# Kernel optimization log

Hardware: AMD Instinct MI355X
Metric: run time of the kernel (lower is better)

## Reference

```python
import math
import jax, jax.numpy as jnp
import numpy as np

B, S, D, H = 2, 2048, 1024, 16
DH = D // H
DFF = 4 * D
EPS = 1e-6
MASKED_BIAS = -10000.0


def _gelu(x):
    # GPT-2 tanh-approx GELU
    return 0.5 * x * (1.0 + jnp.tanh(math.sqrt(2.0 / math.pi) * (x + 0.044715 * x ** 3)))


def _layernorm(x, w, b):
    mean = jnp.mean(x, axis=-1, keepdims=True)
    var = jnp.mean((x - mean) ** 2, axis=-1, keepdims=True)
    return w * ((x - mean) / jnp.sqrt(var + EPS)) + b


def setup_inputs() -> dict:
    key = jax.random.key(0)
    ks = jax.random.split(key, 6)
    std = 0.02
    return {
        "hidden_states": jax.random.normal(ks[0], (B, S, D), jnp.float32),
        "w_attn": jax.random.normal(ks[1], (D, 3 * D), jnp.float32) * std,
        "b_attn": jnp.zeros((3 * D,), jnp.float32),
        "w_proj": jax.random.normal(ks[2], (D, D), jnp.float32) * std,
        "b_proj": jnp.zeros((D,), jnp.float32),
        "w_fc": jax.random.normal(ks[3], (D, DFF), jnp.float32) * std,
        "b_fc": jnp.zeros((DFF,), jnp.float32),
        "w_fc_proj": jax.random.normal(ks[4], (DFF, D), jnp.float32) * std,
        "b_fc_proj": jnp.zeros((D,), jnp.float32),
        "ln1_w": jnp.ones((D,), jnp.float32),
        "ln1_b": jnp.zeros((D,), jnp.float32),
        "ln2_w": jnp.ones((D,), jnp.float32),
        "ln2_b": jnp.zeros((D,), jnp.float32),
    }


def reference(hidden_states, w_attn, b_attn, w_proj, b_proj, w_fc, b_fc,
              w_fc_proj, b_fc_proj, ln1_w, ln1_b, ln2_w, ln2_b):
    residual = hidden_states
    x = _layernorm(hidden_states, ln1_w, ln1_b)

    # c_attn: [B,S,D] @ [D,3D] + b -> split into q,k,v
    qkv = x @ w_attn + b_attn
    q, k, v = jnp.split(qkv, 3, axis=-1)
    # split heads -> [B,H,S,DH]
    q = q.reshape(B, S, H, DH).transpose(0, 2, 1, 3)
    k = k.reshape(B, S, H, DH).transpose(0, 2, 1, 3)
    v = v.reshape(B, S, H, DH).transpose(0, 2, 1, 3)

    scores = jnp.einsum('bhqd,bhkd->bhqk', q, k) / jnp.sqrt(jnp.float32(DH))
    causal = jnp.tril(jnp.ones((S, S), bool))  # [S,S]
    scores = jnp.where(causal[None, None], scores, jnp.float32(MASKED_BIAS))
    attn = jax.nn.softmax(scores, axis=-1)
    out = jnp.einsum('bhqk,bhkd->bhqd', attn, v)
    out = out.transpose(0, 2, 1, 3).reshape(B, S, D)
    out = out @ w_proj + b_proj

    h = residual + out
    residual = h
    y = _layernorm(h, ln2_w, ln2_b)
    y = _gelu(y @ w_fc + b_fc)
    y = y @ w_fc_proj + b_fc_proj
    return residual + y
```

## Files before the change

kernel.cpp:

```cpp
#include <hip/hip_runtime.h>
#include <cstdint>
#include <cstddef>

typedef unsigned short u16;
typedef float  floatx4 __attribute__((ext_vector_type(4)));
typedef short  short8  __attribute__((ext_vector_type(8)));
typedef u16    usx4    __attribute__((ext_vector_type(4)));
typedef u16    usx8    __attribute__((ext_vector_type(8)));

__device__ __forceinline__ u16 f2b(float f) {
  unsigned u = __float_as_uint(f);
  unsigned r = u + 0x7fffu + ((u >> 16) & 1u);
  return (u16)(r >> 16);
}
__device__ __forceinline__ float b2f(u16 s) {
  return __uint_as_float(((unsigned)s) << 16);
}

__device__ __forceinline__ float gelu_f(float x) {
  const float c = 0.7978845608028654f;
  float t = tanhf(c * (x + 0.044715f * x * x * x));
  return 0.5f * x * (1.0f + t);
}

__device__ __forceinline__ void gl2lds16(const u16* g, u16* l) {
  __builtin_amdgcn_global_load_lds(
      (const __attribute__((address_space(1))) unsigned int*)g,
      (__attribute__((address_space(3))) unsigned int*)l, 16, 0, 0);
}

__global__ __launch_bounds__(256) void ln_bf16_kernel(
    const float* __restrict__ in, const float* __restrict__ w,
    const float* __restrict__ b, u16* __restrict__ out)
{
  const int row = blockIdx.x;
  const int t = threadIdx.x;
  const float* p = in + (size_t)row * 1024 + t * 4;
  floatx4 v = *(const floatx4*)p;
  float s  = v.x + v.y + v.z + v.w;
  float ss = v.x*v.x + v.y*v.y + v.z*v.z + v.w*v.w;
  #pragma unroll
  for (int m = 1; m < 64; m <<= 1) {
    s  += __shfl_xor(s,  m);
    ss += __shfl_xor(ss, m);
  }
  __shared__ float red[8];
  if ((t & 63) == 0) { red[(t >> 6)*2] = s; red[(t >> 6)*2 + 1] = ss; }
  __syncthreads();
  s  = red[0] + red[2] + red[4] + red[6];
  ss = red[1] + red[3] + red[5] + red[7];
  const float mean = s * (1.0f / 1024.0f);
  const float var  = ss * (1.0f / 1024.0f) - mean * mean;
  const float rstd = rsqrtf(var + 1e-6f);
  floatx4 wv = *(const floatx4*)(w + t * 4);
  floatx4 bv = *(const floatx4*)(b + t * 4);
  usx4 o = { f2b(wv.x * ((v.x - mean) * rstd) + bv.x),
             f2b(wv.y * ((v.y - mean) * rstd) + bv.y),
             f2b(wv.z * ((v.z - mean) * rstd) + bv.z),
             f2b(wv.w * ((v.w - mean) * rstd) + bv.w) };
  *(usx4*)(out + (size_t)row * 1024 + t * 4) = o;
}

__global__ __launch_bounds__(256) void wtrans_kernel(
    const float* __restrict__ in, u16* __restrict__ out, int K, int N)
{
  __shared__ u16 tile[32][33];
  const int n0 = blockIdx.x * 32, k0 = blockIdx.y * 32;
  const int tx = threadIdx.x & 31, ty = threadIdx.x >> 5;
  #pragma unroll
  for (int i = 0; i < 4; ++i)
    tile[ty + i*8][tx] = f2b(in[(size_t)(k0 + ty + i*8) * N + n0 + tx]);
  __syncthreads();
  #pragma unroll
  for (int i = 0; i < 4; ++i)
    out[(size_t)(n0 + ty + i*8) * K + k0 + tx] = tile[tx][ty + i*8];
}

template<int BM, int BN, int FLAGS, int MINW>
__global__ __launch_bounds__(256, MINW) void gemm_mfma_kernel(
    const u16* __restrict__ A, const u16* __restrict__ Bt,
    const float* __restrict__ bias, const float* __restrict__ Res,
    void* __restrict__ Cout, int M, int N, int K, int kLen)
{
  constexpr int WM = BM / 2, WN = BN / 2;
  constexpr int MT = WM / 16, NT = WN / 16;
  __shared__ u16 As[BM * 32];
  __shared__ u16 Bs[BN * 32];

  const int t = threadIdx.x;
  const int wave = t >> 6, lane = t & 63;
  const int quad = lane >> 4, l16 = lane & 15;
  const int wm = wave >> 1, wn = wave & 1;
  const int bm0 = blockIdx.y * BM, bn0 = blockIdx.x * BN;
  const int kStart = blockIdx.z * kLen;

  const int sRow = lane >> 2;
  const int sq   = lane & 3;

  const u16* aG[BM / 64];
  u16* aL[BM / 64];
  #pragma unroll
  for (int j = 0; j < BM / 64; ++j) {
    const int band = j * 4 + wave;
    aG[j] = A + (size_t)(bm0 + band * 16 + sRow) * K + kStart + sq * 8;
    aL[j] = As + band * 512;
  }
  const u16* bG[BN / 64];
  u16* bL[BN / 64];
  #pragma unroll
  for (int j = 0; j < BN / 64; ++j) {
    const int band = j * 4 + wave;
    bG[j] = Bt + (size_t)(bn0 + band * 16 + sRow) * K + kStart + sq * 8;
    bL[j] = Bs + band * 512;
  }

  floatx4 acc[MT][NT] = {};

  for (int k0 = 0; k0 < kLen; k0 += 32) {
    __syncthreads();
    #pragma unroll
    for (int j = 0; j < BM / 64; ++j) gl2lds16(aG[j] + k0, aL[j]);
    #pragma unroll
    for (int j = 0; j < BN / 64; ++j) gl2lds16(bG[j] + k0, bL[j]);
    __syncthreads();

    short8 af[MT], bf[NT];
    #pragma unroll
    for (int mt = 0; mt < MT; ++mt)
      af[mt] = *(const short8*)&As[(wm*WM + mt*16 + l16) * 32 + quad * 8];
    #pragma unroll
    for (int nt = 0; nt < NT; ++nt)
      bf[nt] = *(const short8*)&Bs[(wn*WN + nt*16 + l16) * 32 + quad * 8];
    #pragma unroll
    for (int mt = 0; mt < MT; ++mt)
      #pragma unroll
      for (int nt = 0; nt < NT; ++nt)
        acc[mt][nt] = __builtin_amdgcn_mfma_f32_16x16x32_bf16(af[mt], bf[nt], acc[mt][nt], 0, 0, 0);
  }

  const int orow0 = bm0 + wm * WM;
  const int ocol0 = bn0 + wn * WN;
  const size_t zoff = (size_t)blockIdx.z * M * N;
  #pragma unroll
  for (int nt = 0; nt < NT; ++nt) {
    const int col = ocol0 + nt*16 + l16;
    const float bv = bias ? bias[col] : 0.0f;
    #pragma unroll
    for (int mt = 0; mt < MT; ++mt) {
      #pragma unroll
      for (int r = 0; r < 4; ++r) {
        const int row = orow0 + mt*16 + quad*4 + r;
        float v = acc[mt][nt][r] + bv;
        if (FLAGS & 1) v = gelu_f(v);
        if (FLAGS & 2) v += Res[(size_t)row * N + col];
        if (FLAGS & 4) ((u16*)Cout)[zoff + (size_t)row * N + col] = f2b(v);
        else           ((float*)Cout)[zoff + (size_t)row * N + col] = v;
      }
    }
  }
}

__global__ __launch_bounds__(256, 4) void attn_mfma_kernel(
    const u16* __restrict__ qkv, u16* __restrict__ opart, float* __restrict__ ml)
{
  __shared__ u16 Ks[64][72];
  __shared__ u16 Vt[64][72];
  __shared__ u16 Ps[64][72];

  const int t    = threadIdx.x;
  const int wave = t >> 6;
  const int lane = t & 63;
  const int quad = lane >> 4;
  const int l16  = lane & 15;
  const int pair = blockIdx.x >> 1;
  const int half = blockIdx.x & 1;
  const int h    = blockIdx.y;
  const int b    = blockIdx.z;

  const size_t base = (size_t)b * 2048 * 3072;
  const int qoff = h * 64;
  const int koff = 1024 + h * 64;
  const int voff = 2048 + h * 64;

  const int srow = t >> 2;
  const int scol = (t & 3) * 16;
  const int kpair  = t & 31;
  const int vchunk = t >> 5;

  const size_t obase  = ((((size_t)half * 2 + b) * 16 + h) * 2048) * 64;
  const size_t mlbase = ((((size_t)half * 2 + b) * 16 + h) * 2048) * 2;

  const float C2 = 0.18033688011112042f;

  #pragma unroll 1
  for (int iter = 0; iter < 2; ++iter) {
    const int qi = iter ? (31 - pair) : pair;
    const int q0 = qi << 6;
    const int T  = qi + 1;
    const int mid = (T + 1) >> 1;
    const int t0 = half ? mid : 0;
    const int t1 = half ? T : mid;

    floatx4 of[4] = {};
    float m[4], l[4];
    #pragma unroll
    for (int r = 0; r < 4; ++r) { m[r] = -1e30f; l[r] = 0.f; }

    if (t0 < t1) {
      __syncthreads();
      {
        const u16* qp = qkv + base + (size_t)(q0 + srow) * 3072 + qoff + scol;
        *(usx8*)&Ks[srow][scol]     = *(const usx8*)qp;
        *(usx8*)&Ks[srow][scol + 8] = *(const usx8*)(qp + 8);
      }
      __syncthreads();
      const short8 qf0 = *(const short8*)&Ks[wave*16 + l16][quad*8];
      const short8 qf1 = *(const short8*)&Ks[wave*16 + l16][32 + quad*8];

      usx8 kr0, kr1, vr0, vr1;
      {
        const int k0 = t0 << 6;
        const u16* kp = qkv + base + (size_t)(k0 + srow) * 3072 + koff + scol;
        kr0 = *(const usx8*)kp; kr1 = *(const usx8*)(kp + 8);
        const u16* vp = qkv + base + (size_t)(k0 + 2*kpair) * 3072 + voff + vchunk*8;
        vr0 = *(const usx8*)vp; vr1 = *(const usx8*)(vp + 3072);
      }

      for (int tIdx = t0; tIdx < t1; ++tIdx) {
        __syncthreads();
        *(usx8*)&Ks[srow][scol]     = kr0;
        *(usx8*)&Ks[srow][scol + 8] = kr1;
        #pragma unroll
        for (int i = 0; i < 8; ++i)
          *(unsigned*)&Vt[vchunk*8 + i][2*kpair] =
              (unsigned)vr0[i] | ((unsigned)vr1[i] << 16);
        __syncthreads();

        if (tIdx + 1 < t1) {
          const int kn = (tIdx + 1) << 6;
          const u16* kp = qkv + base + (size_t)(kn + srow) * 3072 + koff + scol;
          kr0 = *(const usx8*)kp; kr1 = *(const usx8*)(kp + 8);
          const u16* vp = qkv + base + (size_t)(kn + 2*kpair) * 3072 + voff + vchunk*8;
          vr0 = *(const usx8*)vp; vr1 = *(const usx8*)(vp + 3072);
        }

        const int k0 = tIdx << 6;
        floatx4 sf[4];
        #pragma unroll
        for (int kt = 0; kt < 4; ++kt) {
          short8 kf0 = *(const short8*)&Ks[kt*16 + l16][quad*8];
          short8 kf1 = *(const short8*)&Ks[kt*16 + l16][32 + quad*8];
          floatx4 z = {};
          z      = __builtin_amdgcn_mfma_f32_16x16x32_bf16(qf0, kf0, z, 0, 0, 0);
          sf[kt] = __builtin_amdgcn_mfma_f32_16x16x32_bf16(qf1, kf1, z, 0, 0, 0);
        }

        const bool diag = (tIdx == qi);
        #pragma unroll
        for (int r = 0; r < 4; ++r) {
          const int qrow = q0 + wave*16 + quad*4 + r;
          float sv[4];
          #pragma unroll
          for (int kt = 0; kt < 4; ++kt) {
            sv[kt] = sf[kt][r] * C2;
            if (diag && (k0 + kt*16 + l16 > qrow)) sv[kt] = -1e30f;
          }
          float mx = fmaxf(fmaxf(sv[0], sv[1]), fmaxf(sv[2], sv[3]));
          #pragma unroll
          for (int msk = 1; msk < 16; msk <<= 1) mx = fmaxf(mx, __shfl_xor(mx, msk));
          const float nm = fmaxf(m[r], mx);
          float rs = 0.f;
          u16 pb[4];
          #pragma unroll
          for (int kt = 0; kt < 4; ++kt) {
            pb[kt] = f2b(exp2f(sv[kt] - nm));
            rs += b2f(pb[kt]);
          }
          #pragma unroll
          for (int msk = 1; msk < 16; msk <<= 1) rs += __shfl_xor(rs, msk);
          const float alpha = exp2f(m[r] - nm);
          m[r] = nm;
          l[r] = l[r] * alpha + rs;
          #pragma unroll
          for (int dht = 0; dht < 4; ++dht) of[dht][r] *= alpha;
          #pragma unroll
          for (int kt = 0; kt < 4; ++kt)
            Ps[wave*16 + quad*4 + r][kt*16 + l16] = pb[kt];
        }

        short8 pf0 = *(const short8*)&Ps[wave*16 + l16][quad*8];
        short8 pf1 = *(const short8*)&Ps[wave*16 + l16][32 + quad*8];
        #pragma unroll
        for (int dht = 0; dht < 4; ++dht) {
          short8 vf0 = *(const short8*)&Vt[dht*16 + l16][quad*8];
          short8 vf1 = *(const short8*)&Vt[dht*16 + l16][32 + quad*8];
          of[dht] = __builtin_amdgcn_mfma_f32_16x16x32_bf16(pf0, vf0, of[dht], 0, 0, 0);
          of[dht] = __builtin_amdgcn_mfma_f32_16x16x32_bf16(pf1, vf1, of[dht], 0, 0, 0);
        }
      }
    }

    #pragma unroll
    for (int r = 0; r < 4; ++r) {
      const int s = q0 + wave*16 + quad*4 + r;
      u16* orow = opart + obase + (size_t)s * 64;
      #pragma unroll
      for (int dht = 0; dht < 4; ++dht) orow[dht*16 + l16] = f2b(of[dht][r]);
      if (l16 == 0) { ml[mlbase + 2*s] = m[r]; ml[mlbase + 2*s + 1] = l[r]; }
    }
  }
}

__global__ __launch_bounds__(256) void attn_combine_kernel(
    const u16* __restrict__ opart, const float* __restrict__ ml,
    u16* __restrict__ out)
{
  const int t = threadIdx.x;
  const int s = blockIdx.x * 4 + (t >> 6);
  const int lane = t & 63;
  const int h = blockIdx.y, b = blockIdx.z;

  const size_t o0  = ((((size_t)0 * 2 + b) * 16 + h) * 2048 + s) * 64 + lane;
  const size_t o1  = ((((size_t)1 * 2 + b) * 16 + h) * 2048 + s) * 64 + lane;
  const size_t ml0 = ((((size_t)0 * 2 + b) * 16 + h) * 2048 + s) * 2;
  const size_t ml1 = ((((size_t)1 * 2 + b) * 16 + h) * 2048 + s) * 2;

  const float m0 = ml[ml0], l0 = ml[ml0 + 1];
  const float m1 = ml[ml1], l1 = ml[ml1 + 1];
  const float M  = fmaxf(m0, m1);
  const float w0 = exp2f(m0 - M), w1 = exp2f(m1 - M);
  const float L  = w0 * l0 + w1 * l1;
  const float o  = w0 * b2f(opart[o0]) + w1 * b2f(opart[o1]);
  out[((size_t)b * 2048 + s) * 1024 + h * 64 + lane] = f2b(o / L);
}

__global__ __launch_bounds__(256) void fcproj_combine_kernel(
    const u16* __restrict__ p, const float* __restrict__ hbuf,
    const float* __restrict__ bias, float* __restrict__ out)
{
  const size_t i0 = ((size_t)blockIdx.x * 256 + threadIdx.x) * 8;
  usx8 a = *(const usx8*)(p + i0);
  usx8 c = *(const usx8*)(p + 4194304 + i0);
  const int col = (int)(i0 & 1023);
  floatx4 bv0 = *(const floatx4*)(bias + col);
  floatx4 bv1 = *(const floatx4*)(bias + col + 4);
  floatx4 h0 = *(const floatx4*)(hbuf + i0);
  floatx4 h1 = *(const floatx4*)(hbuf + i0 + 4);
  floatx4 o0, o1;
  #pragma unroll
  for (int i = 0; i < 4; ++i) o0[i] = h0[i] + b2f(a[i])   + b2f(c[i])   + bv0[i];
  #pragma unroll
  for (int i = 0; i < 4; ++i) o1[i] = h1[i] + b2f(a[4+i]) + b2f(c[4+i]) + bv1[i];
  *(floatx4*)(out + i0)     = o0;
  *(floatx4*)(out + i0 + 4) = o1;
}

extern "C" void kernel_launch(void* const* d_in, const int* in_sizes, int n_in,
                              void* d_out, int out_size, void* d_ws, size_t ws_size,
                              hipStream_t stream) {
  const float* hidden    = (const float*)d_in[0];
  const float* w_attn    = (const float*)d_in[1];
  const float* b_attn    = (const float*)d_in[2];
  const float* w_proj    = (const float*)d_in[3];
  const float* b_proj    = (const float*)d_in[4];
  const float* w_fc      = (const float*)d_in[5];
  const float* b_fc      = (const float*)d_in[6];
  const float* w_fc_proj = (const float*)d_in[7];
  const float* b_fc_proj = (const float*)d_in[8];
  const float* ln1_w     = (const float*)d_in[9];
  const float* ln1_b     = (const float*)d_in[10];
  const float* ln2_w     = (const float*)d_in[11];
  const float* ln2_b     = (const float*)d_in[12];

  char* wsb = (char*)d_ws;
  u16*   xb    = (u16*)  (wsb + (size_t)( 0u << 20));
  u16*   qkvb  = (u16*)  (wsb + (size_t)( 8u << 20));
  u16*   attnb = (u16*)  (wsb + (size_t)(32u << 20));
  float* hbuf  = (float*)(wsb + (size_t)(40u << 20));
  u16*   opart = (u16*)  (wsb + (size_t)(40u << 20));
  float* mlbuf = (float*)(wsb + (size_t)(56u << 20));
  u16*   wqT   = (u16*)  (wsb + (size_t)(56u << 20));
  u16*   wpT   = (u16*)  (wsb + (size_t)(62u << 20));
  u16*   wfT   = (u16*)  (wsb + (size_t)(64u << 20));
  u16*   wfpT  = (u16*)  (wsb + (size_t)(72u << 20));
  u16*   pfcp  = (u16*)  (wsb + (size_t)(56u << 20));
  u16*   fcb   = qkvb;
  u16*   yb    = xb;

  wtrans_kernel<<<dim3(96, 32),  256, 0, stream>>>(w_attn,    wqT,  1024, 3072);
  wtrans_kernel<<<dim3(32, 32),  256, 0, stream>>>(w_proj,    wpT,  1024, 1024);
  wtrans_kernel<<<dim3(128, 32), 256, 0, stream>>>(w_fc,      wfT,  1024, 4096);
  wtrans_kernel<<<dim3(32, 128), 256, 0, stream>>>(w_fc_proj, wfpT, 4096, 1024);

  ln_bf16_kernel<<<4096, 256, 0, stream>>>(hidden, ln1_w, ln1_b, xb);
  gemm_mfma_kernel<128,128,4,4><<<dim3(24, 32, 1), 256, 0, stream>>>(
      xb, wqT, b_attn, nullptr, qkvb, 4096, 3072, 1024, 1024);
  attn_mfma_kernel<<<dim3(32, 16, 2), 256, 0, stream>>>(qkvb, opart, mlbuf);
  attn_combine_kernel<<<dim3(512, 16, 2), 256, 0, stream>>>(opart, mlbuf, attnb);
  gemm_mfma_kernel<128,64,2,4><<<dim3(16, 32, 1), 256, 0, stream>>>(
      attnb, wpT, b_proj, hidden, hbuf, 4096, 1024, 1024, 1024);
  ln_bf16_kernel<<<4096, 256, 0, stream>>>(hbuf, ln2_w, ln2_b, yb);
  gemm_mfma_kernel<256,128,5,2><<<dim3(32, 16, 1), 256, 0, stream>>>(
      yb, wfT, b_fc, nullptr, fcb, 4096, 4096, 1024, 1024);
  gemm_mfma_kernel<128,64,4,4><<<dim3(16, 32, 2), 256, 0, stream>>>(
      fcb, wfpT, nullptr, nullptr, pfcp, 4096, 1024, 4096, 2048);
  fcproj_combine_kernel<<<dim3(2048), 256, 0, stream>>>(pfcp, hbuf, b_fc_proj, (float*)d_out);
}
```

Measured before the change: 405.7 us.

## Fold softmax scale into QKV GEMM, compute row sums via MFMA, retile fc_proj

The Q-column scaling by log2(e)/sqrt(dh) moves into the QKV GEMM epilogue (flag 8), so the attention kernel no longer multiplies every score. The per-row softmax denominators are now accumulated by an extra MFMA of P against a ones vector, replacing the shuffle-reduced sum, and the max reduction uses width-16 shuffles. The fc_proj GEMM switches to 128x128 tiles with half as many column blocks. This trims VALU and cross-lane work in the attention inner loop at the cost of two extra MFMAs per tile and a small extra multiply in the GEMM epilogue.

```diff
diff --git a/kernel.cpp b/kernel.cpp
--- a/kernel.cpp
+++ b/kernel.cpp
@@ -28,6 +28,8 @@
       (const __attribute__((address_space(1))) unsigned int*)g,
       (__attribute__((address_space(3))) unsigned int*)l, 16, 0, 0);
 }
+
+#define C2SCALE 0.18033688011112042f
 
 __global__ __launch_bounds__(256) void ln_bf16_kernel(
     const float* __restrict__ in, const float* __restrict__ w,
@@ -145,6 +147,7 @@
   for (int nt = 0; nt < NT; ++nt) {
     const int col = ocol0 + nt*16 + l16;
     const float bv = bias ? bias[col] : 0.0f;
+    const float postscale = ((FLAGS & 8) && col < 1024) ? C2SCALE : 1.0f;
     #pragma unroll
     for (int mt = 0; mt < MT; ++mt) {
       #pragma unroll
@@ -152,6 +155,7 @@
         const int row = orow0 + mt*16 + quad*4 + r;
         float v = acc[mt][nt][r] + bv;
         if (FLAGS & 1) v = gelu_f(v);
+        if (FLAGS & 8) v *= postscale;
         if (FLAGS & 2) v += Res[(size_t)row * N + col];
         if (FLAGS & 4) ((u16*)Cout)[zoff + (size_t)row * N + col] = f2b(v);
         else           ((float*)Cout)[zoff + (size_t)row * N + col] = v;
@@ -190,7 +194,12 @@
   const size_t obase  = ((((size_t)half * 2 + b) * 16 + h) * 2048) * 64;
   const size_t mlbase = ((((size_t)half * 2 + b) * 16 + h) * 2048) * 2;
 
-  const float C2 = 0.18033688011112042f;
+  short8 onesb;
+  {
+    const short v = (l16 == 0) ? (short)0x3F80 : (short)0;
+    #pragma unroll
+    for (int i = 0; i < 8; ++i) onesb[i] = v;
+  }
 
   #pragma unroll 1
   for (int iter = 0; iter < 2; ++iter) {
@@ -202,9 +211,10 @@
     const int t1 = half ? T : mid;
 
     floatx4 of[4] = {};
-    float m[4], l[4];
-    #pragma unroll
-    for (int r = 0; r < 4; ++r) { m[r] = -1e30f; l[r] = 0.f; }
+    floatx4 ofl = {};
+    float m[4];
+    #pragma unroll
+    for (int r = 0; r < 4; ++r) m[r] = -1e30f;
 
     if (t0 < t1) {
       __syncthreads();
@@ -258,34 +268,27 @@
         const bool diag = (tIdx == qi);
         #pragma unroll
         for (int r = 0; r < 4; ++r) {
-          const int qrow = q0 + wave*16 + quad*4 + r;
-          float sv[4];
+          float sv0 = sf[0][r], sv1 = sf[1][r], sv2 = sf[2][r], sv3 = sf[3][r];
+          if (diag) {
+            const int qrow = q0 + wave*16 + quad*4 + r;
+            if (k0 +      l16 > qrow) sv0 = -1e30f;
+            if (k0 + 16 + l16 > qrow) sv1 = -1e30f;
+            if (k0 + 32 + l16 > qrow) sv2 = -1e30f;
+            if (k0 + 48 + l16 > qrow) sv3 = -1e30f;
+          }
+          float mx = fmaxf(fmaxf(sv0, sv1), fmaxf(sv2, sv3));
           #pragma unroll
-          for (int kt = 0; kt < 4; ++kt) {
-            sv[kt] = sf[kt][r] * C2;
-            if (diag && (k0 + kt*16 + l16 > qrow)) sv[kt] = -1e30f;
-          }
-          float mx = fmaxf(fmaxf(sv[0], sv[1]), fmaxf(sv[2], sv[3]));
-          #pragma unroll
-          for (int msk = 1; msk < 16; msk <<= 1) mx = fmaxf(mx, __shfl_xor(mx, msk));
+          for (int msk = 1; msk < 16; msk <<= 1) mx = fmaxf(mx, __shfl_xor(mx, msk, 16));
           const float nm = fmaxf(m[r], mx);
-          float rs = 0.f;
-          u16 pb[4];
-          #pragma unroll
-          for (int kt = 0; kt < 4; ++kt) {
-            pb[kt] = f2b(exp2f(sv[kt] - nm));
-            rs += b2f(pb[kt]);
-          }
-          #pragma unroll
-          for (int msk = 1; msk < 16; msk <<= 1) rs += __shfl_xor(rs, msk);
           const float alpha = exp2f(m[r] - nm);
           m[r] = nm;
-          l[r] = l[r] * alpha + rs;
+          Ps[wave*16 + quad*4 + r][     l16] = f2b(exp2f(sv0 - nm));
+          Ps[wave*16 + quad*4 + r][16 + l16] = f2b(exp2f(sv1 - nm));
+          Ps[wave*16 + quad*4 + r][32 + l16] = f2b(exp2f(sv2 - nm));
+          Ps[wave*16 + quad*4 + r][48 + l16] = f2b(exp2f(sv3 - nm));
           #pragma unroll
           for (int dht = 0; dht < 4; ++dht) of[dht][r] *= alpha;
-          #pragma unroll
-          for (int kt = 0; kt < 4; ++kt)
-            Ps[wave*16 + quad*4 + r][kt*16 + l16] = pb[kt];
+          ofl[r] *= alpha;
         }
 
         short8 pf0 = *(const short8*)&Ps[wave*16 + l16][quad*8];
@@ -297,6 +300,8 @@
           of[dht] = __builtin_amdgcn_mfma_f32_16x16x32_bf16(pf0, vf0, of[dht], 0, 0, 0);
           of[dht] = __builtin_amdgcn_mfma_f32_16x16x32_bf16(pf1, vf1, of[dht], 0, 0, 0);
         }
+        ofl = __builtin_amdgcn_mfma_f32_16x16x32_bf16(pf0, onesb, ofl, 0, 0, 0);
+        ofl = __builtin_amdgcn_mfma_f32_16x16x32_bf16(pf1, onesb, ofl, 0, 0, 0);
       }
     }
 
@@ -306,7 +311,8 @@
       u16* orow = opart + obase + (size_t)s * 64;
       #pragma unroll
       for (int dht = 0; dht < 4; ++dht) orow[dht*16 + l16] = f2b(of[dht][r]);
-      if (l16 == 0) { ml[mlbase + 2*s] = m[r]; ml[mlbase + 2*s + 1] = l[r]; }
+      const float lr = __shfl(ofl[r], quad * 16);
+      if (l16 == 0) { ml[mlbase + 2*s] = m[r]; ml[mlbase + 2*s + 1] = lr; }
     }
   }
 }
@@ -335,7 +341,7 @@
 }
 
 __global__ __launch_bounds__(256) void fcproj_combine_kernel(
-    const u16* __restrict__ p, const float* __restrict__ hbuf,
+    const u16* __restrict__ p, const float* __restrict__ res,
     const float* __restrict__ bias, float* __restrict__ out)
 {
   const size_t i0 = ((size_t)blockIdx.x * 256 + threadIdx.x) * 8;
@@ -344,8 +350,8 @@
   const int col = (int)(i0 & 1023);
   floatx4 bv0 = *(const floatx4*)(bias + col);
   floatx4 bv1 = *(const floatx4*)(bias + col + 4);
-  floatx4 h0 = *(const floatx4*)(hbuf + i0);
-  floatx4 h1 = *(const floatx4*)(hbuf + i0 + 4);
+  floatx4 h0 = *(const floatx4*)(res + i0);
+  floatx4 h1 = *(const floatx4*)(res + i0 + 4);
   floatx4 o0, o1;
   #pragma unroll
   for (int i = 0; i < 4; ++i) o0[i] = h0[i] + b2f(a[i])   + b2f(c[i])   + bv0[i];
@@ -393,7 +399,7 @@
   wtrans_kernel<<<dim3(32, 128), 256, 0, stream>>>(w_fc_proj, wfpT, 4096, 1024);
 
   ln_bf16_kernel<<<4096, 256, 0, stream>>>(hidden, ln1_w, ln1_b, xb);
-  gemm_mfma_kernel<128,128,4,4><<<dim3(24, 32, 1), 256, 0, stream>>>(
+  gemm_mfma_kernel<128,128,12,4><<<dim3(24, 32, 1), 256, 0, stream>>>(
       xb, wqT, b_attn, nullptr, qkvb, 4096, 3072, 1024, 1024);
   attn_mfma_kernel<<<dim3(32, 16, 2), 256, 0, stream>>>(qkvb, opart, mlbuf);
   attn_combine_kernel<<<dim3(512, 16, 2), 256, 0, stream>>>(opart, mlbuf, attnb);
@@ -402,7 +408,7 @@
   ln_bf16_kernel<<<4096, 256, 0, stream>>>(hbuf, ln2_w, ln2_b, yb);
   gemm_mfma_kernel<256,128,5,2><<<dim3(32, 16, 1), 256, 0, stream>>>(
       yb, wfT, b_fc, nullptr, fcb, 4096, 4096, 1024, 1024);
-  gemm_mfma_kernel<128,64,4,4><<<dim3(16, 32, 2), 256, 0, stream>>>(
+  gemm_mfma_kernel<128,128,4,4><<<dim3(8, 32, 2), 256, 0, stream>>>(
       fcb, wfpT, nullptr, nullptr, pfcp, 4096, 1024, 4096, 2048);
   fcproj_combine_kernel<<<dim3(2048), 256, 0, stream>>>(pfcp, hbuf, b_fc_proj, (float*)d_out);
 }
```

After: 386.7 us. -4.7%, faster.
